# Performance work log

Measured on AMD Instinct MI355X. Metric: run time of the kernel, lower is better.

Reference implementation:

```python
import jax, jax.numpy as jnp
import numpy as np

EPS = 1e-6
N_LEVELS = 8
BASE_RES = 16
DESIRED_RES = 128
N_POINTS = 524288


def _grid_meta():
    # replicate DAGrid.__init__ level resolutions and flat-table offsets
    b = (DESIRED_RES / BASE_RES) ** (1.0 / (N_LEVELS - 1))
    scales, offsets = [], [0]
    for i in range(N_LEVELS):
        res = int(BASE_RES * b ** i)
        scales.append(res)
        offsets.append(offsets[-1] + (res + 1) ** 3)
    return scales, offsets


def setup_inputs() -> dict:
    key = jax.random.key(0)
    scales, offsets = _grid_meta()
    lo = np.array([-1.0, -1.0, -1.0], np.float32)
    hi_eps = np.array([1.0, 1.0, 1.0], np.float32) - EPS  # bounds[1] -= eps before anchor init
    anchors = []
    for res in scales:
        axes = [np.linspace(lo[d], hi_eps[d], res + 1, dtype=np.float32) for d in range(3)]
        g = np.stack(np.meshgrid(*axes, indexing='ij'), axis=-1).reshape(-1, 3)
        anchors.append(g)
    data = jnp.asarray(np.concatenate(anchors, axis=0))  # (T, 3) learned grid param
    xyz = jax.random.normal(key, (N_POINTS, 3), dtype=jnp.float32)
    return {
        'xyz': xyz,
        'data': data,
        'scales': jnp.asarray(scales, jnp.float32),              # (L,)
        'level_offsets': jnp.asarray(offsets[:-1], jnp.int32),   # (L,)
        'bounds': jnp.asarray(np.stack([lo, np.array([1.0, 1.0, 1.0], np.float32)])),  # (2,3) raw bbox
    }


def reference(xyz, data, scales, level_offsets, bounds):
    L = scales.shape[0]
    lo = bounds[0]
    hi = bounds[1] - EPS
    size = jnp.max(bounds[1] - bounds[0])
    x = jnp.clip(xyz, lo, hi)
    xn = (x - lo) / size                                   # (N,3) in [0,1)
    fx = xn[None, :, :] * scales[:, None, None]            # (L,N,3)
    base = jnp.floor(fx).astype(jnp.int32)                 # (L,N,3) lower corner
    off = fx - base.astype(fx.dtype)                       # (L,N,3) trilinear frac
    corners = jnp.asarray([[0, 0, 0], [0, 0, 1], [0, 1, 0], [0, 1, 1],
                           [1, 0, 0], [1, 0, 1], [1, 1, 0], [1, 1, 1]], jnp.int32)  # (8,3)
    idx = base[:, :, None, :] + corners[None, None, :, :]  # (L,N,8,3)
    r1 = (scales + 1.0).astype(jnp.int32)                  # (L,) points per axis
    ind = (idx[..., 0] * (r1 * r1)[:, None, None]
           + idx[..., 1] * r1[:, None, None]
           + idx[..., 2]
           + level_offsets[:, None, None])                 # (L,N,8) flat gather index
    val = data[ind]                                        # (L,N,8,3) gathered anchors
    cf = corners.astype(fx.dtype)
    w = jnp.clip(1.0 - cf + (2.0 * cf - 1.0) * off[:, :, None, :], 0.0, 1.0)  # (L,N,8,3)
    w = w[..., 0] * w[..., 1] * w[..., 2]                  # (L,N,8) trilinear weights
    freqs = (2.0 ** jnp.arange(L, dtype=fx.dtype))[:, None, None, None]
    enc = jnp.concatenate([jnp.sin(val * freqs), jnp.cos(val * freqs)], axis=-1)  # (L,N,8,6)
    out = jnp.einsum('lnk,lnkf->nlf', w, enc)              # (N,L,6)
    out = out.reshape(xyz.shape[0], -1)                    # (N, 6*L)
    return jnp.concatenate([xyz, out], axis=-1)            # (N, 3 + 6*L)
```

## Files before the change

### kernel.cpp

```cpp
#include <hip/hip_runtime.h>

#define NLEV 8
#define PTS_PER_BLOCK 32
#define ROW_F 51

typedef float f4u __attribute__((ext_vector_type(4), aligned(4)));
typedef float f2u __attribute__((ext_vector_type(2), aligned(4)));

__global__ __launch_bounds__(256) void dagrid_kernel(
    const float* __restrict__ xyz,
    const float* __restrict__ data,
    const float* __restrict__ scales,
    const int*   __restrict__ level_offsets,
    const float* __restrict__ bounds,
    float* __restrict__ out,
    int npts)
{
    __shared__ alignas(16) float sxyz[PTS_PER_BLOCK * 3];
    __shared__ alignas(16) float sres[PTS_PER_BLOCK][ROW_F];

    const int tid = threadIdx.x;
    const int l   = tid & 7;
    const int p   = tid >> 3;
    const int block_base = blockIdx.x * PTS_PER_BLOCK;
    const bool full_block = (block_base + PTS_PER_BLOCK <= npts);

    if (full_block) {
        if (tid < 24) {
            ((float4*)sxyz)[tid] = ((const float4*)(xyz + (size_t)block_base * 3))[tid];
        }
    } else if (tid < PTS_PER_BLOCK * 3) {
        const int gi = block_base * 3 + tid;
        sxyz[tid] = (gi < npts * 3) ? xyz[gi] : 0.0f;
    }

    const float scale = scales[l];
    const int   off_l = level_offsets[l];

    const float lox = bounds[0], loy = bounds[1], loz = bounds[2];
    const float hix = bounds[3] - 1e-6f;
    const float hiy = bounds[4] - 1e-6f;
    const float hiz = bounds[5] - 1e-6f;
    const float size = fmaxf(fmaxf(bounds[3] - bounds[0], bounds[4] - bounds[1]),
                             bounds[5] - bounds[2]);
    const float inv_size = 1.0f / size;

    __syncthreads();

    const int n = block_base + p;
    const bool active = (n < npts);

    const float rx = sxyz[p * 3 + 0];
    const float ry = sxyz[p * 3 + 1];
    const float rz = sxyz[p * 3 + 2];

    float acc0 = 0.f, acc1 = 0.f, acc2 = 0.f, acc3 = 0.f, acc4 = 0.f, acc5 = 0.f;

    if (active) {
        const float x = fminf(fmaxf(rx, lox), hix);
        const float y = fminf(fmaxf(ry, loy), hiy);
        const float z = fminf(fmaxf(rz, loz), hiz);
        const float xn = (x - lox) * inv_size;
        const float yn = (y - loy) * inv_size;
        const float zn = (z - loz) * inv_size;

        const int r1   = (int)scale + 1;
        const int r1sq = r1 * r1;

        const float fx = xn * scale;
        const float fy = yn * scale;
        const float fz = zn * scale;
        const float bxf = floorf(fx), byf = floorf(fy), bzf = floorf(fz);
        const float ox = fx - bxf;
        const float oy = fy - byf;
        const float oz = fz - bzf;

        const int i000 = (int)bxf * r1sq + (int)byf * r1 + (int)bzf + off_l;

        const float* p0 = data + 3 * (size_t)i000;
        const float* p1 = p0 + 3 * r1;
        const float* p2 = p0 + 3 * r1sq;
        const float* p3 = p2 + 3 * r1;

        const f4u a0 = *(const f4u*)p0;  const f2u b0 = *(const f2u*)(p0 + 4);
        const f4u a1 = *(const f4u*)p1;  const f2u b1 = *(const f2u*)(p1 + 4);
        const f4u a2 = *(const f4u*)p2;  const f2u b2 = *(const f2u*)(p2 + 4);
        const f4u a3 = *(const f4u*)p3;  const f2u b3 = *(const f2u*)(p3 + 4);

        const float freq = (float)(1 << l);
        const float wz0  = 1.0f - oz;
        const float wx1 = ox, wx0 = 1.0f - ox;
        const float wy1 = oy, wy0 = 1.0f - oy;

        float sn, cs;
        #define PAIR(a, b, WXY)                                                   \
        {                                                                         \
            const float w0 = (WXY) * wz0;                                         \
            const float w1 = (WXY) * oz;                                          \
            __sincosf(a.x * freq, &sn, &cs); acc0 += w0 * sn; acc3 += w0 * cs;    \
            __sincosf(a.y * freq, &sn, &cs); acc1 += w0 * sn; acc4 += w0 * cs;    \
            __sincosf(a.z * freq, &sn, &cs); acc2 += w0 * sn; acc5 += w0 * cs;    \
            __sincosf(a.w * freq, &sn, &cs); acc0 += w1 * sn; acc3 += w1 * cs;    \
            __sincosf(b.x * freq, &sn, &cs); acc1 += w1 * sn; acc4 += w1 * cs;    \
            __sincosf(b.y * freq, &sn, &cs); acc2 += w1 * sn; acc5 += w1 * cs;    \
        }
        PAIR(a0, b0, wx0 * wy0)
        PAIR(a1, b1, wx0 * wy1)
        PAIR(a2, b2, wx1 * wy0)
        PAIR(a3, b3, wx1 * wy1)
        #undef PAIR
    }

    {
        float* row = sres[p];
        const int c = 3 + l * 6;
        row[c + 0] = acc0; row[c + 1] = acc1; row[c + 2] = acc2;
        row[c + 3] = acc3; row[c + 4] = acc4; row[c + 5] = acc5;
        if (l == 0) { row[0] = rx; row[1] = ry; row[2] = rz; }
    }
    __syncthreads();

    if (full_block) {
        const float4* flat4 = (const float4*)&sres[0][0];
        float4* ob4 = (float4*)(out + (size_t)block_base * ROW_F);
        for (int i = tid; i < (PTS_PER_BLOCK * ROW_F) / 4; i += 256)
            ob4[i] = flat4[i];
    } else {
        const float* flat = &sres[0][0];
        float* ob = out + (size_t)block_base * ROW_F;
        const int lim = npts * ROW_F - block_base * ROW_F;
        for (int i = tid; i < PTS_PER_BLOCK * ROW_F; i += 256)
            if (i < lim) ob[i] = flat[i];
    }
}

extern "C" void kernel_launch(void* const* d_in, const int* in_sizes, int n_in,
                              void* d_out, int out_size, void* d_ws, size_t ws_size,
                              hipStream_t stream) {
    const float* xyz           = (const float*)d_in[0];
    const float* data          = (const float*)d_in[1];
    const float* scales        = (const float*)d_in[2];
    const int*   level_offsets = (const int*)d_in[3];
    const float* bounds        = (const float*)d_in[4];
    float* out = (float*)d_out;

    const int npts = in_sizes[0] / 3;
    const int nblocks = (npts + PTS_PER_BLOCK - 1) / PTS_PER_BLOCK;
    dagrid_kernel<<<nblocks, 256, 0, stream>>>(xyz, data, scales, level_offsets,
                                               bounds, out, npts);
}
```

Baseline: 142.2 us.

## Stage corner gathers through shared memory with cooperative 12-byte loads

Each thread now computes its four corner-pair base addresses and writes them to shared memory. After a barrier, the whole block cooperatively gathers the 8 corners per (point, level) as 3-float loads into a shared staging buffer, then each thread reads its 24 values back from LDS for the sincos accumulation. The aim is to reorganize the scattered global gathers so that adjacent lanes issue loads from nearby addresses, improving coalescing. In exchange it adds two extra barriers and roughly 28KB of LDS per block, which may reduce occupancy, and the strided SLOT=26 layout may cause LDS bank conflicts.

```diff
diff --git a/kernel.cpp b/kernel.cpp
--- a/kernel.cpp
+++ b/kernel.cpp
@@ -3,9 +3,10 @@
 #define NLEV 8
 #define PTS_PER_BLOCK 32
 #define ROW_F 51
+#define UNITS 256
+#define SLOT 26
 
-typedef float f4u __attribute__((ext_vector_type(4), aligned(4)));
-typedef float f2u __attribute__((ext_vector_type(2), aligned(4)));
+typedef float f3u __attribute__((ext_vector_type(3), aligned(4)));
 
 __global__ __launch_bounds__(256) void dagrid_kernel(
     const float* __restrict__ xyz,
@@ -17,6 +18,8 @@
     int npts)
 {
     __shared__ alignas(16) float sxyz[PTS_PER_BLOCK * 3];
+    __shared__ unsigned         saddr[UNITS * 4];
+    __shared__ alignas(16) float spair[UNITS * SLOT];
     __shared__ alignas(16) float sres[PTS_PER_BLOCK][ROW_F];
 
     const int tid = threadIdx.x;
@@ -54,9 +57,8 @@
     const float ry = sxyz[p * 3 + 1];
     const float rz = sxyz[p * 3 + 2];
 
-    float acc0 = 0.f, acc1 = 0.f, acc2 = 0.f, acc3 = 0.f, acc4 = 0.f, acc5 = 0.f;
-
-    if (active) {
+    float ox = 0.f, oy = 0.f, oz = 0.f;
+    {
         const float x = fminf(fmaxf(rx, lox), hix);
         const float y = fminf(fmaxf(ry, loy), hiy);
         const float z = fminf(fmaxf(rz, loz), hiz);
@@ -71,44 +73,61 @@
         const float fy = yn * scale;
         const float fz = zn * scale;
         const float bxf = floorf(fx), byf = floorf(fy), bzf = floorf(fz);
-        const float ox = fx - bxf;
-        const float oy = fy - byf;
-        const float oz = fz - bzf;
+        ox = fx - bxf;
+        oy = fy - byf;
+        oz = fz - bzf;
 
         const int i000 = (int)bxf * r1sq + (int)byf * r1 + (int)bzf + off_l;
+        const unsigned b0 = active ? 3u * (unsigned)i000 : 0u;
+        saddr[tid * 4 + 0] = b0;
+        saddr[tid * 4 + 1] = active ? b0 + 3u * (unsigned)r1 : 0u;
+        saddr[tid * 4 + 2] = active ? b0 + 3u * (unsigned)r1sq : 0u;
+        saddr[tid * 4 + 3] = active ? b0 + 3u * (unsigned)(r1sq + r1) : 0u;
+    }
 
-        const float* p0 = data + 3 * (size_t)i000;
-        const float* p1 = p0 + 3 * r1;
-        const float* p2 = p0 + 3 * r1sq;
-        const float* p3 = p2 + 3 * r1;
+    __syncthreads();
 
-        const f4u a0 = *(const f4u*)p0;  const f2u b0 = *(const f2u*)(p0 + 4);
-        const f4u a1 = *(const f4u*)p1;  const f2u b1 = *(const f2u*)(p1 + 4);
-        const f4u a2 = *(const f4u*)p2;  const f2u b2 = *(const f2u*)(p2 + 4);
-        const f4u a3 = *(const f4u*)p3;  const f2u b3 = *(const f2u*)(p3 + 4);
+    #pragma unroll
+    for (int k = 0; k < 8; ++k) {
+        const int m = tid + 256 * k;
+        const int q = m >> 1;
+        const int h = m & 1;
+        const unsigned gidx = saddr[q] + 3u * (unsigned)h;
+        const f3u v = *(const f3u*)(data + gidx);
+        const int u = q >> 2;
+        const int c = q & 3;
+        float* dst = &spair[u * SLOT + c * 6 + 3 * h];
+        dst[0] = v.x; dst[1] = v.y; dst[2] = v.z;
+    }
 
+    __syncthreads();
+
+    float acc0 = 0.f, acc1 = 0.f, acc2 = 0.f, acc3 = 0.f, acc4 = 0.f, acc5 = 0.f;
+    if (active) {
         const float freq = (float)(1 << l);
         const float wz0  = 1.0f - oz;
         const float wx1 = ox, wx0 = 1.0f - ox;
         const float wy1 = oy, wy0 = 1.0f - oy;
+        const float* up = &spair[tid * SLOT];
 
         float sn, cs;
-        #define PAIR(a, b, WXY)                                                   \
+        #define PAIRC(c, WXY)                                                     \
         {                                                                         \
             const float w0 = (WXY) * wz0;                                         \
             const float w1 = (WXY) * oz;                                          \
-            __sincosf(a.x * freq, &sn, &cs); acc0 += w0 * sn; acc3 += w0 * cs;    \
-            __sincosf(a.y * freq, &sn, &cs); acc1 += w0 * sn; acc4 += w0 * cs;    \
-            __sincosf(a.z * freq, &sn, &cs); acc2 += w0 * sn; acc5 += w0 * cs;    \
-            __sincosf(a.w * freq, &sn, &cs); acc0 += w1 * sn; acc3 += w1 * cs;    \
-            __sincosf(b.x * freq, &sn, &cs); acc1 += w1 * sn; acc4 += w1 * cs;    \
-            __sincosf(b.y * freq, &sn, &cs); acc2 += w1 * sn; acc5 += w1 * cs;    \
+            const float* pv = up + (c) * 6;                                       \
+            __sincosf(pv[0] * freq, &sn, &cs); acc0 += w0 * sn; acc3 += w0 * cs;  \
+            __sincosf(pv[1] * freq, &sn, &cs); acc1 += w0 * sn; acc4 += w0 * cs;  \
+            __sincosf(pv[2] * freq, &sn, &cs); acc2 += w0 * sn; acc5 += w0 * cs;  \
+            __sincosf(pv[3] * freq, &sn, &cs); acc0 += w1 * sn; acc3 += w1 * cs;  \
+            __sincosf(pv[4] * freq, &sn, &cs); acc1 += w1 * sn; acc4 += w1 * cs;  \
+            __sincosf(pv[5] * freq, &sn, &cs); acc2 += w1 * sn; acc5 += w1 * cs;  \
         }
-        PAIR(a0, b0, wx0 * wy0)
-        PAIR(a1, b1, wx0 * wy1)
-        PAIR(a2, b2, wx1 * wy0)
-        PAIR(a3, b3, wx1 * wy1)
-        #undef PAIR
+        PAIRC(0, wx0 * wy0)
+        PAIRC(1, wx0 * wy1)
+        PAIRC(2, wx1 * wy0)
+        PAIRC(3, wx1 * wy1)
+        #undef PAIRC
     }
 
     {
```

Measured after the change: 138.9 us. 2.3% less time.

## Precompute quantized per-anchor phase table and use hardware revolution-based sin/cos

Applied to the files above, without the earlier changes.

Adds a repack kernel that, for each grid anchor, stores the frequency-scaled phase of the anchor and its +z neighbour as 16-bit fixed-point fractions of a revolution, packed into one uint4. The main kernel then does four 16-byte gathers instead of eight unaligned vector loads and calls v_sin_f32/v_cos_f32 directly, with no range reduction or frequency multiply. The aim is lower gather traffic and a cheaper transcendental path. In exchange it adds an extra launch over the whole table each call and quantizes phase to 16 bits, which reduces accuracy.

```diff
diff --git a/kernel.cpp b/kernel.cpp
--- a/kernel.cpp
+++ b/kernel.cpp
@@ -4,10 +4,172 @@
 #define PTS_PER_BLOCK 32
 #define ROW_F 51
 
+__global__ __launch_bounds__(256) void phase_repack(
+    const float* __restrict__ data,
+    const int*   __restrict__ level_offsets,
+    uint4* __restrict__ tab, int T)
+{
+    __shared__ float sv[(256 + 1) * 3];
+    __shared__ int   soff[NLEV];
+    const int tid  = threadIdx.x;
+    const int base = blockIdx.x * 256;
+
+    if (tid < NLEV) soff[tid] = level_offsets[tid];
+    for (int k = tid; k < (256 + 1) * 3; k += 256) {
+        const int gi = base * 3 + k;
+        sv[k] = (gi < T * 3) ? data[gi] : 0.0f;
+    }
+    __syncthreads();
+
+    const int i = base + tid;
+    if (i >= T) return;
+
+    int l = 0;
+    #pragma unroll
+    for (int j = 1; j < NLEV; ++j) l += (i >= soff[j]) ? 1 : 0;
+    const float s = exp2f((float)l) * 0.15915494309189535f;
+
+    unsigned q[6];
+    #pragma unroll
+    for (int k = 0; k < 6; ++k) {
+        float f = sv[tid * 3 + k] * s;
+        f -= floorf(f);
+        const unsigned v = (unsigned)(f * 65536.0f + 0.5f);
+        q[k] = v & 0xffffu;
+    }
+    tab[i] = make_uint4(q[0] | (q[1] << 16), q[2], q[3] | (q[4] << 16), q[5]);
+}
+
+__device__ __forceinline__ void sincos_rev(float r, float& sn, float& cs) {
+    asm volatile("v_sin_f32 %0, %1" : "=v"(sn) : "v"(r));
+    asm volatile("v_cos_f32 %0, %1" : "=v"(cs) : "v"(r));
+}
+
+__global__ __launch_bounds__(256) void dagrid_kernel(
+    const float* __restrict__ xyz,
+    const uint4* __restrict__ tab,
+    const float* __restrict__ scales,
+    const int*   __restrict__ level_offsets,
+    const float* __restrict__ bounds,
+    float* __restrict__ out,
+    int npts)
+{
+    __shared__ alignas(16) float sxyz[PTS_PER_BLOCK * 3];
+    __shared__ alignas(16) float sres[PTS_PER_BLOCK][ROW_F];
+
+    const int tid = threadIdx.x;
+    const int l   = tid & 7;
+    const int p   = tid >> 3;
+    const int block_base = blockIdx.x * PTS_PER_BLOCK;
+    const bool full_block = (block_base + PTS_PER_BLOCK <= npts);
+
+    if (full_block) {
+        if (tid < 24)
+            ((float4*)sxyz)[tid] = ((const float4*)(xyz + (size_t)block_base * 3))[tid];
+    } else if (tid < PTS_PER_BLOCK * 3) {
+        const int gi = block_base * 3 + tid;
+        sxyz[tid] = (gi < npts * 3) ? xyz[gi] : 0.0f;
+    }
+
+    const float scale = scales[l];
+    const int   off_l = level_offsets[l];
+
+    const float lox = bounds[0], loy = bounds[1], loz = bounds[2];
+    const float hix = bounds[3] - 1e-6f;
+    const float hiy = bounds[4] - 1e-6f;
+    const float hiz = bounds[5] - 1e-6f;
+    const float size = fmaxf(fmaxf(bounds[3] - bounds[0], bounds[4] - bounds[1]),
+                             bounds[5] - bounds[2]);
+    const float inv_size = 1.0f / size;
+
+    __syncthreads();
+
+    const int n = block_base + p;
+    const bool active = (n < npts);
+
+    const float rx = sxyz[p * 3 + 0];
+    const float ry = sxyz[p * 3 + 1];
+    const float rz = sxyz[p * 3 + 2];
+
+    float acc0 = 0.f, acc1 = 0.f, acc2 = 0.f, acc3 = 0.f, acc4 = 0.f, acc5 = 0.f;
+
+    if (active) {
+        const float x = fminf(fmaxf(rx, lox), hix);
+        const float y = fminf(fmaxf(ry, loy), hiy);
+        const float z = fminf(fmaxf(rz, loz), hiz);
+        const float xn = (x - lox) * inv_size;
+        const float yn = (y - loy) * inv_size;
+        const float zn = (z - loz) * inv_size;
+
+        const int r1   = (int)scale + 1;
+        const int r1sq = r1 * r1;
+
+        const float fx = xn * scale;
+        const float fy = yn * scale;
+        const float fz = zn * scale;
+        const float bxf = floorf(fx), byf = floorf(fy), bzf = floorf(fz);
+        const float ox = fx - bxf;
+        const float oy = fy - byf;
+        const float oz = fz - bzf;
+
+        const int i000 = (int)bxf * r1sq + (int)byf * r1 + (int)bzf + off_l;
+
+        const uint4 e0 = tab[i000];
+        const uint4 e1 = tab[i000 + r1];
+        const uint4 e2 = tab[i000 + r1sq];
+        const uint4 e3 = tab[i000 + r1sq + r1];
+
+        const float wz0 = 1.0f - oz;
+        const float wx1 = ox, wx0 = 1.0f - ox;
+        const float wy1 = oy, wy0 = 1.0f - oy;
+        const float K = 1.0f / 65536.0f;
+
+        float sn, cs;
+        #define PAIRE(e, WXY)                                                        \
+        {                                                                            \
+            const float w0 = (WXY) * wz0;                                            \
+            const float w1 = (WXY) * oz;                                             \
+            sincos_rev((float)(e.x & 0xffffu) * K, sn, cs); acc0 += w0*sn; acc3 += w0*cs; \
+            sincos_rev((float)(e.x >> 16)     * K, sn, cs); acc1 += w0*sn; acc4 += w0*cs; \
+            sincos_rev((float)(e.y & 0xffffu) * K, sn, cs); acc2 += w0*sn; acc5 += w0*cs; \
+            sincos_rev((float)(e.z & 0xffffu) * K, sn, cs); acc0 += w1*sn; acc3 += w1*cs; \
+            sincos_rev((float)(e.z >> 16)     * K, sn, cs); acc1 += w1*sn; acc4 += w1*cs; \
+            sincos_rev((float)(e.w & 0xffffu) * K, sn, cs); acc2 += w1*sn; acc5 += w1*cs; \
+        }
+        PAIRE(e0, wx0 * wy0)
+        PAIRE(e1, wx0 * wy1)
+        PAIRE(e2, wx1 * wy0)
+        PAIRE(e3, wx1 * wy1)
+        #undef PAIRE
+    }
+
+    {
+        float* row = sres[p];
+        const int c = 3 + l * 6;
+        row[c + 0] = acc0; row[c + 1] = acc1; row[c + 2] = acc2;
+        row[c + 3] = acc3; row[c + 4] = acc4; row[c + 5] = acc5;
+        if (l == 0) { row[0] = rx; row[1] = ry; row[2] = rz; }
+    }
+    __syncthreads();
+
+    if (full_block) {
+        const float4* flat4 = (const float4*)&sres[0][0];
+        float4* ob4 = (float4*)(out + (size_t)block_base * ROW_F);
+        for (int i = tid; i < (PTS_PER_BLOCK * ROW_F) / 4; i += 256)
+            ob4[i] = flat4[i];
+    } else {
+        const float* flat = &sres[0][0];
+        float* ob = out + (size_t)block_base * ROW_F;
+        const int lim = npts * ROW_F - block_base * ROW_F;
+        for (int i = tid; i < PTS_PER_BLOCK * ROW_F; i += 256)
+            if (i < lim) ob[i] = flat[i];
+    }
+}
+
 typedef float f4u __attribute__((ext_vector_type(4), aligned(4)));
 typedef float f2u __attribute__((ext_vector_type(2), aligned(4)));
 
-__global__ __launch_bounds__(256) void dagrid_kernel(
+__global__ __launch_bounds__(256) void dagrid_kernel_direct(
     const float* __restrict__ xyz,
     const float* __restrict__ data,
     const float* __restrict__ scales,
@@ -23,20 +185,13 @@
     const int l   = tid & 7;
     const int p   = tid >> 3;
     const int block_base = blockIdx.x * PTS_PER_BLOCK;
-    const bool full_block = (block_base + PTS_PER_BLOCK <= npts);
-
-    if (full_block) {
-        if (tid < 24) {
-            ((float4*)sxyz)[tid] = ((const float4*)(xyz + (size_t)block_base * 3))[tid];
-        }
-    } else if (tid < PTS_PER_BLOCK * 3) {
+
+    if (tid < PTS_PER_BLOCK * 3) {
         const int gi = block_base * 3 + tid;
         sxyz[tid] = (gi < npts * 3) ? xyz[gi] : 0.0f;
     }
-
     const float scale = scales[l];
     const int   off_l = level_offsets[l];
-
     const float lox = bounds[0], loy = bounds[1], loz = bounds[2];
     const float hix = bounds[3] - 1e-6f;
     const float hiy = bounds[4] - 1e-6f;
@@ -44,16 +199,13 @@
     const float size = fmaxf(fmaxf(bounds[3] - bounds[0], bounds[4] - bounds[1]),
                              bounds[5] - bounds[2]);
     const float inv_size = 1.0f / size;
-
     __syncthreads();
 
     const int n = block_base + p;
     const bool active = (n < npts);
-
     const float rx = sxyz[p * 3 + 0];
     const float ry = sxyz[p * 3 + 1];
     const float rz = sxyz[p * 3 + 2];
-
     float acc0 = 0.f, acc1 = 0.f, acc2 = 0.f, acc3 = 0.f, acc4 = 0.f, acc5 = 0.f;
 
     if (active) {
@@ -63,35 +215,24 @@
         const float xn = (x - lox) * inv_size;
         const float yn = (y - loy) * inv_size;
         const float zn = (z - loz) * inv_size;
-
-        const int r1   = (int)scale + 1;
+        const int r1 = (int)scale + 1;
         const int r1sq = r1 * r1;
-
-        const float fx = xn * scale;
-        const float fy = yn * scale;
-        const float fz = zn * scale;
+        const float fx = xn * scale, fy = yn * scale, fz = zn * scale;
         const float bxf = floorf(fx), byf = floorf(fy), bzf = floorf(fz);
-        const float ox = fx - bxf;
-        const float oy = fy - byf;
-        const float oz = fz - bzf;
-
+        const float ox = fx - bxf, oy = fy - byf, oz = fz - bzf;
         const int i000 = (int)bxf * r1sq + (int)byf * r1 + (int)bzf + off_l;
-
         const float* p0 = data + 3 * (size_t)i000;
         const float* p1 = p0 + 3 * r1;
         const float* p2 = p0 + 3 * r1sq;
         const float* p3 = p2 + 3 * r1;
-
         const f4u a0 = *(const f4u*)p0;  const f2u b0 = *(const f2u*)(p0 + 4);
         const f4u a1 = *(const f4u*)p1;  const f2u b1 = *(const f2u*)(p1 + 4);
         const f4u a2 = *(const f4u*)p2;  const f2u b2 = *(const f2u*)(p2 + 4);
         const f4u a3 = *(const f4u*)p3;  const f2u b3 = *(const f2u*)(p3 + 4);
-
         const float freq = (float)(1 << l);
-        const float wz0  = 1.0f - oz;
+        const float wz0 = 1.0f - oz;
         const float wx1 = ox, wx0 = 1.0f - ox;
         const float wy1 = oy, wy0 = 1.0f - oy;
-
         float sn, cs;
         #define PAIR(a, b, WXY)                                                   \
         {                                                                         \
@@ -110,7 +251,6 @@
         PAIR(a3, b3, wx1 * wy1)
         #undef PAIR
     }
-
     {
         float* row = sres[p];
         const int c = 3 + l * 6;
@@ -119,13 +259,7 @@
         if (l == 0) { row[0] = rx; row[1] = ry; row[2] = rz; }
     }
     __syncthreads();
-
-    if (full_block) {
-        const float4* flat4 = (const float4*)&sres[0][0];
-        float4* ob4 = (float4*)(out + (size_t)block_base * ROW_F);
-        for (int i = tid; i < (PTS_PER_BLOCK * ROW_F) / 4; i += 256)
-            ob4[i] = flat4[i];
-    } else {
+    {
         const float* flat = &sres[0][0];
         float* ob = out + (size_t)block_base * ROW_F;
         const int lim = npts * ROW_F - block_base * ROW_F;
@@ -145,7 +279,18 @@
     float* out = (float*)d_out;
 
     const int npts = in_sizes[0] / 3;
+    const int T    = in_sizes[1] / 3;
     const int nblocks = (npts + PTS_PER_BLOCK - 1) / PTS_PER_BLOCK;
-    dagrid_kernel<<<nblocks, 256, 0, stream>>>(xyz, data, scales, level_offsets,
-                                               bounds, out, npts);
-}
+
+    const size_t ws_needed = (size_t)T * sizeof(uint4);
+    if (d_ws != nullptr && ws_size >= ws_needed) {
+        uint4* tab = (uint4*)d_ws;
+        phase_repack<<<(T + 255) / 256, 256, 0, stream>>>(data, level_offsets, tab, T);
+        dagrid_kernel<<<nblocks, 256, 0, stream>>>(xyz, tab, scales, level_offsets,
+                                                   bounds, out, npts);
+    } else {
+        dagrid_kernel_direct<<<nblocks, 256, 0, stream>>>(xyz, data, scales,
+                                                          level_offsets, bounds,
+                                                          out, npts);
+    }
+}
```

Result: slower. 153.1 us (+7.7%).
